# Performance work log

Measured on AMD Instinct MI355X. Metric: run time of the kernel, lower is better.

The kernel has to match this reference:

```python
import jax, jax.numpy as jnp
import numpy as np

G, T, S, M = 128, 512, 24, 4


def setup_inputs() -> dict:
    key = jax.random.key(0)
    k0, k1, k2, k3, k4 = jax.random.split(key, 5)
    inp = jax.random.normal(k0, (G, T, M), dtype=jnp.float32)
    # Stable-ish transition matrices: near 0.95*I
    F = 0.95 * jnp.eye(S, dtype=jnp.float32) + 0.05 * jax.random.normal(k1, (G, T, S, S), dtype=jnp.float32) / jnp.sqrt(S)
    # PSD process noise Q = c*A A^T + eps*I
    Aq = jax.random.normal(k2, (G, T, S, S), dtype=jnp.float32)
    Q = (0.01 / S) * jnp.einsum('gtik,gtjk->gtij', Aq, Aq) + 1e-3 * jnp.eye(S, dtype=jnp.float32)
    H = 0.5 * jax.random.normal(k3, (G, T, M, S), dtype=jnp.float32)
    # PSD measurement noise R
    Ar = jax.random.normal(k4, (G, T, M, M), dtype=jnp.float32)
    R = (0.1 / M) * jnp.einsum('gtik,gtjk->gtij', Ar, Ar) + 1e-2 * jnp.eye(M, dtype=jnp.float32)
    init_mean = jnp.zeros((G, S), dtype=jnp.float32)
    init_cov = jnp.broadcast_to(jnp.eye(S, dtype=jnp.float32), (G, S, S))
    return dict(input=inp, F=F, Q=Q, H=H, R=R, init_mean=init_mean, init_cov=init_cov)


def _measure(m, P, Hc, Rc):
    # one-step-ahead measurement distribution: mu = H m, Sig = H P H^T + R
    mu = jnp.einsum('gms,gs->gm', Hc, m)
    Sig = Hc @ P @ Hc.swapaxes(-1, -2) + Rc
    return mu, Sig


def _kalman(input, F, Q, H, R, init_mean, init_cov):
    # time-major for scan
    y = jnp.moveaxis(input, 1, 0)      # [T,G,M]
    Ft = jnp.moveaxis(F, 1, 0)         # [T,G,S,S]
    Qt = jnp.moveaxis(Q, 1, 0)
    Ht = jnp.moveaxis(H, 1, 0)         # [T,G,M,S]
    Rt = jnp.moveaxis(R, 1, 0)         # [T,G,M,M]

    mu0, Sig0 = _measure(init_mean, init_cov, Ht[0], Rt[0])

    def step(carry, x):
        m, P = carry                     # state prediction for t-1: [G,S], [G,S,S]
        yprev, Fp, Qp, Hp, Rp, Hc, Rc = x
        # --- update with obs at t-1 (using H,R from the t-1 measurement) ---
        HP = Hp @ P                      # [G,M,S]
        Sm = HP @ Hp.swapaxes(-1, -2) + Rp   # innovation cov [G,M,M]
        # K = P H^T S^{-1}; using symmetry: K = solve(S, H P)^T
        K = jnp.linalg.solve(Sm, HP).swapaxes(-1, -2)  # [G,S,M]
        resid = yprev - jnp.einsum('gms,gs->gm', Hp, m)
        m_u = m + jnp.einsum('gsm,gm->gs', K, resid)
        P_u = P - K @ HP
        # --- predict to t ---
        m_p = jnp.einsum('gij,gj->gi', Fp, m_u)
        P_p = Fp @ P_u @ Fp.swapaxes(-1, -2) + Qp
        # --- measurement at t ---
        mu, Sig = _measure(m_p, P_p, Hc, Rc)
        return (m_p, P_p), (mu, Sig)

    xs = (y[:-1], Ft[:-1], Qt[:-1], Ht[:-1], Rt[:-1], Ht[1:], Rt[1:])
    _, (mus, Sigs) = jax.lax.scan(step, (init_mean, init_cov), xs)
    means = jnp.moveaxis(jnp.concatenate([mu0[None], mus], axis=0), 0, 1)   # [G,T,M]
    covs = jnp.moveaxis(jnp.concatenate([Sig0[None], Sigs], axis=0), 0, 1)  # [G,T,M,M]
    return means, covs


def reference(input, F, Q, H, R, init_mean, init_cov):
    return _kalman(input, F, Q, H, R, init_mean, init_cov)
```

## Files before the change

kernel.cpp:

```cpp
#include <hip/hip_runtime.h>

#define Gn 128
#define Tn 512
#define Sn 24
#define SP 28
#define Mn 4
#define COVS_BASE (Gn * Tn * Mn)

__device__ __forceinline__ float4 ld4(const float* p) {
    return *reinterpret_cast<const float4*>(p);
}
__device__ __forceinline__ void st4(float* p, float4 v) {
    *reinterpret_cast<float4*>(p) = v;
}
__device__ __forceinline__ float dot4(float4 a, float4 b) {
    return a.x*b.x + a.y*b.y + a.z*b.z + a.w*b.w;
}

struct Row24 { float4 v[6]; };

__device__ __forceinline__ Row24 loadRow(const float* p) {
    Row24 r;
#pragma unroll
    for (int i = 0; i < 6; ++i) r.v[i] = ld4(p + 4*i);
    return r;
}

__device__ __forceinline__ float dot24(const Row24& a, const float* b) {
    float4 b0 = ld4(b+0), b1 = ld4(b+4), b2 = ld4(b+8),
           b3 = ld4(b+12), b4 = ld4(b+16), b5 = ld4(b+20);
    float s0 = a.v[0].x*b0.x + a.v[0].y*b0.y + a.v[0].z*b0.z + a.v[0].w*b0.w;
    float s1 = a.v[1].x*b1.x + a.v[1].y*b1.y + a.v[1].z*b1.z + a.v[1].w*b1.w;
    float s2 = a.v[2].x*b2.x + a.v[2].y*b2.y + a.v[2].z*b2.z + a.v[2].w*b2.w;
    float s3 = a.v[3].x*b3.x + a.v[3].y*b3.y + a.v[3].z*b3.z + a.v[3].w*b3.w;
    float s4 = a.v[4].x*b4.x + a.v[4].y*b4.y + a.v[4].z*b4.z + a.v[4].w*b4.w;
    float s5 = a.v[5].x*b5.x + a.v[5].y*b5.y + a.v[5].z*b5.z + a.v[5].w*b5.w;
    return ((s0+s1)+(s2+s3))+(s4+s5);
}

__device__ __forceinline__ void barrierLds() {
    asm volatile("s_waitcnt lgkmcnt(0)" ::: "memory");
    __builtin_amdgcn_s_barrier();
    asm volatile("" ::: "memory");
}
__device__ __forceinline__ void waveLds() {
    asm volatile("s_waitcnt lgkmcnt(0)" ::: "memory");
    __builtin_amdgcn_wave_barrier();
    asm volatile("" ::: "memory");
}

extern "C" __global__ void __launch_bounds__(256)
kalman_kernel(const float* __restrict__ y_g, const float* __restrict__ F_g,
              const float* __restrict__ Q_g, const float* __restrict__ H_g,
              const float* __restrict__ R_g, const float* __restrict__ m0_g,
              const float* __restrict__ P0_g, float* __restrict__ out)
{
    const int g   = blockIdx.x;
    const int tid = threadIdx.x;
    const int gT  = g * Tn;

    __shared__ __align__(16) float sP[Sn*SP];
    __shared__ __align__(16) float sPu[Sn*SP];
    __shared__ __align__(16) float sTmp[Sn*SP];
    __shared__ __align__(16) float sF[2][Sn*SP];
    __shared__ __align__(16) float sQ[2][Sn*SP];
    __shared__ __align__(16) float sH[2][Mn*SP];
    __shared__ __align__(16) float sR[2][16];
    __shared__ __align__(16) float sy[2][4];
    __shared__ __align__(16) float sHP[Mn*SP];
    __shared__ __align__(16) float sHPT[Sn*4];
    __shared__ __align__(16) float sK[Sn*4];
    __shared__ __align__(16) float sSig[16];
    __shared__ __align__(16) float sInv[16];
    __shared__ __align__(16) float sMean[Sn];
    __shared__ __align__(16) float sMu_[Sn];
    __shared__ __align__(16) float sResid[4];

    const float4* F4 = reinterpret_cast<const float4*>(F_g);
    const float4* Q4 = reinterpret_cast<const float4*>(Q_g);
    const float4* H4 = reinterpret_cast<const float4*>(H_g);
    const float4* R4 = reinterpret_cast<const float4*>(R_g);
    const float4* y4 = reinterpret_cast<const float4*>(y_g);

    auto stage_load = [&](int v, int t) -> float4 {
        if (v < 144)      return F4[(gT + t)*144 + v];
        else if (v < 288) return Q4[(gT + t)*144 + (v-144)];
        else if (v < 312) return H4[(gT + t)*24  + (v-288)];
        else if (v < 316) return R4[(gT + t)*4   + (v-312)];
        else              return y4[gT + t];
    };
    auto stage_store = [&](int v, int bb, float4 val) {
        if (v < 144)      { int r = v/6,        c = (v%6)*4;       st4(&sF[bb][r*SP+c], val); }
        else if (v < 288) { int v2 = v-144; int r = v2/6, c = (v2%6)*4; st4(&sQ[bb][r*SP+c], val); }
        else if (v < 312) { int v2 = v-288; int r = v2/6, c = (v2%6)*4; st4(&sH[bb][r*SP+c], val); }
        else if (v < 316) { st4(&sR[bb][(v-312)*4], val); }
        else              { st4(&sy[bb][0], val); }
    };

    if (tid < 144) {
        int r = tid / 6, c = (tid % 6) * 4;
        st4(&sP[r*SP + c], ld4(&P0_g[g*Sn*Sn + tid*4]));
    } else if (tid < 150) {
        int v = tid - 144;
        st4(&sMean[v*4], ld4(&m0_g[g*Sn + v*4]));
    }
    {
        float4 a0 = stage_load(tid, 0);
        stage_store(tid, 0, a0);
        if (tid + 256 < 317) {
            float4 a1 = stage_load(tid + 256, 0);
            stage_store(tid + 256, 0, a1);
        }
    }
    barrierLds();

    float4 pf0, pf1;

    for (int t = 0; t < Tn; ++t) {
        const int  b    = t & 1;
        const int  b1   = b ^ 1;
        const bool last = (t == Tn - 1);

        if (!last) {
            pf0 = stage_load(tid, t+1);
            if (tid + 256 < 317) pf1 = stage_load(tid + 256, t+1);
        }
        if (tid < 96) {
            int a = tid / 24, s = tid % 24;
            Row24 hr = loadRow(&sH[b][a*SP]);
            float hp = dot24(hr, &sP[s*SP]);
            sHP[a*SP + s]  = hp;
            sHPT[s*4 + a]  = hp;
        } else if (tid >= 128 && tid < 132) {
            int a = tid - 128;
            Row24 hr = loadRow(&sH[b][a*SP]);
            float mu = dot24(hr, sMean);
            out[(gT + t)*4 + a] = mu;
            sResid[a] = sy[b][a] - mu;
        }
        barrierLds();

        if (tid < 64) {
            if (tid < 16) {
                int a = tid >> 2, c = tid & 3;
                Row24 hpr = loadRow(&sHP[a*SP]);
                float sig = dot24(hpr, &sH[b][c*SP]) + sR[b][tid];
                sSig[tid] = sig;
                out[COVS_BASE + (size_t)(gT + t)*16 + tid] = sig;
            }
            if (!last) {
                waveLds();
                if (tid < 16) {
                    float s00=sSig[0],  s01=sSig[1],  s02=sSig[2],  s03=sSig[3];
                    float s10=sSig[4],  s11=sSig[5],  s12=sSig[6],  s13=sSig[7];
                    float s20=sSig[8],  s21=sSig[9],  s22=sSig[10], s23=sSig[11];
                    float s30=sSig[12], s31=sSig[13], s32=sSig[14], s33=sSig[15];
                    float p0 = s00*s11 - s01*s10;
                    float p1 = s00*s12 - s02*s10;
                    float p2 = s00*s13 - s03*s10;
                    float p3 = s01*s12 - s02*s11;
                    float p4 = s01*s13 - s03*s11;
                    float p5 = s02*s13 - s03*s12;
                    float q0c = s20*s31 - s21*s30;
                    float q1c = s20*s32 - s22*s30;
                    float q2c = s20*s33 - s23*s30;
                    float q3c = s21*s32 - s22*s31;
                    float q4c = s21*s33 - s23*s31;
                    float q5c = s22*s33 - s23*s32;
                    float det  = p0*q5c - p1*q4c + p2*q3c + p3*q2c - p4*q1c + p5*q0c;
                    float rdet = 1.0f / det;
                    int ia = tid >> 2, ic = tid & 3;
                    int r0 = (ic==0)?1:0, r1 = (ic<=1)?2:1, r2 = (ic<=2)?3:2;
                    int u0 = (ia==0)?1:0, u1 = (ia<=1)?2:1, u2 = (ia<=2)?3:2;
                    float m00=sSig[r0*4+u0], m01=sSig[r0*4+u1], m02=sSig[r0*4+u2];
                    float m10=sSig[r1*4+u0], m11=sSig[r1*4+u1], m12=sSig[r1*4+u2];
                    float m20=sSig[r2*4+u0], m21=sSig[r2*4+u1], m22=sSig[r2*4+u2];
                    float minor = m00*(m11*m22 - m12*m21)
                                - m01*(m10*m22 - m12*m20)
                                + m02*(m10*m21 - m11*m20);
                    float cof = ((ia + ic) & 1) ? -minor : minor;
                    sInv[tid] = cof * rdet;
                }
                waveLds();
                {
                    int a = tid / 24, s = tid % 24;
                    float kt = dot4(ld4(&sInv[a*4]), ld4(&sHPT[s*4]));
                    sK[s*4 + a] = kt;
                    if (tid < 32) {
                        int o2 = 64 + tid, a3 = o2/24, s3 = o2%24;
                        float kt2 = dot4(ld4(&sInv[a3*4]), ld4(&sHPT[s3*4]));
                        sK[s3*4 + a3] = kt2;
                    }
                }
            }
        }
        if (last) return;
        barrierLds();

        {
            int o = 2*tid, i = o/24, j = o%24;
            float4 kr = ld4(&sK[i*4]);
            float pu0 = sP[i*SP+j]   - dot4(kr, ld4(&sHPT[j*4]));
            float pu1 = sP[i*SP+j+1] - dot4(kr, ld4(&sHPT[(j+1)*4]));
            sPu[i*SP+j]   = pu0;
            sPu[i*SP+j+1] = pu1;
            if (tid >= 64 && tid < 128) {
                int o2 = 512 + (tid-64), i2 = o2/24, j2 = o2%24;
                sPu[i2*SP+j2] = sP[i2*SP+j2] - dot4(ld4(&sK[i2*4]), ld4(&sHPT[j2*4]));
            }
            if (tid >= 192 && tid < 216) {
                int s = tid - 192;
                sMu_[s] = sMean[s] + dot4(ld4(&sK[s*4]), ld4(&sResid[0]));
            }
        }
        barrierLds();

        {
            int o = 2*tid, i = o/24, j = o%24;
            Row24 fr = loadRow(&sF[b][i*SP]);
            sTmp[i*SP+j]   = dot24(fr, &sPu[j*SP]);
            sTmp[i*SP+j+1] = dot24(fr, &sPu[(j+1)*SP]);
            if (tid >= 64 && tid < 128) {
                int o2 = 512 + (tid-64), i2 = o2/24, j2 = o2%24;
                Row24 fr2 = loadRow(&sF[b][i2*SP]);
                sTmp[i2*SP+j2] = dot24(fr2, &sPu[j2*SP]);
            }
            if (tid >= 224 && tid < 248) {
                int i3 = tid - 224;
                Row24 fr3 = loadRow(&sF[b][i3*SP]);
                sMean[i3] = dot24(fr3, sMu_);
            }
        }
        barrierLds();

        {
            int o = 2*tid, i = o/24, j = o%24;
            Row24 tr = loadRow(&sTmp[i*SP]);
            sP[i*SP+j]   = dot24(tr, &sF[b][j*SP])     + sQ[b][i*SP+j];
            sP[i*SP+j+1] = dot24(tr, &sF[b][(j+1)*SP]) + sQ[b][i*SP+j+1];
            if (tid >= 64 && tid < 128) {
                int o2 = 512 + (tid-64), i2 = o2/24, j2 = o2%24;
                Row24 tr2 = loadRow(&sTmp[i2*SP]);
                sP[i2*SP+j2] = dot24(tr2, &sF[b][j2*SP]) + sQ[b][i2*SP+j2];
            }
            stage_store(tid, b1, pf0);
            if (tid + 256 < 317) stage_store(tid + 256, b1, pf1);
        }
        barrierLds();
    }
}

extern "C" void kernel_launch(void* const* d_in, const int* in_sizes, int n_in,
                              void* d_out, int out_size, void* d_ws, size_t ws_size,
                              hipStream_t stream) {
    kalman_kernel<<<Gn, 256, 0, stream>>>(
        (const float*)d_in[0], (const float*)d_in[1], (const float*)d_in[2],
        (const float*)d_in[3], (const float*)d_in[4], (const float*)d_in[5],
        (const float*)d_in[6], (float*)d_out);
}
```

Measured before the change: 1.282 ms.

## Reformulate Kalman step algebraically to cut per-step barriers from five to three

Rewrites the covariance update as F P F^T + Q - V S^{-1} V^T, where V = F P H^T, and the mean update as F m + V S^{-1} resid. This removes the explicit gain K and the intermediate P_u/Tmp matrices. F·P is now computed alongside H·P, and V, F·m and the 4x4 inverse are computed in parallel on different waves. The goal is to cut barrier-separated phases per time step and shorten the serial dependency chain. It changes the floating-point ordering of the covariance update and could be slightly less numerically stable than the Joseph-free K form.

```diff
diff --git a/kernel.cpp b/kernel.cpp
--- a/kernel.cpp
+++ b/kernel.cpp
@@ -60,21 +60,20 @@
     const int gT  = g * Tn;
 
     __shared__ __align__(16) float sP[Sn*SP];
-    __shared__ __align__(16) float sPu[Sn*SP];
-    __shared__ __align__(16) float sTmp[Sn*SP];
+    __shared__ __align__(16) float sG[Sn*SP];
     __shared__ __align__(16) float sF[2][Sn*SP];
     __shared__ __align__(16) float sQ[2][Sn*SP];
     __shared__ __align__(16) float sH[2][Mn*SP];
     __shared__ __align__(16) float sR[2][16];
     __shared__ __align__(16) float sy[2][4];
     __shared__ __align__(16) float sHP[Mn*SP];
-    __shared__ __align__(16) float sHPT[Sn*4];
-    __shared__ __align__(16) float sK[Sn*4];
-    __shared__ __align__(16) float sSig[16];
+    __shared__ __align__(16) float sV[Sn*4];
+    __shared__ __align__(16) float sSm[16];
     __shared__ __align__(16) float sInv[16];
     __shared__ __align__(16) float sMean[Sn];
-    __shared__ __align__(16) float sMu_[Sn];
+    __shared__ __align__(16) float sFm[Sn];
     __shared__ __align__(16) float sResid[4];
+    __shared__ __align__(16) float sr2[4];
 
     const float4* F4 = reinterpret_cast<const float4*>(F_g);
     const float4* Q4 = reinterpret_cast<const float4*>(Q_g);
@@ -90,7 +89,7 @@
         else              return y4[gT + t];
     };
     auto stage_store = [&](int v, int bb, float4 val) {
-        if (v < 144)      { int r = v/6,        c = (v%6)*4;       st4(&sF[bb][r*SP+c], val); }
+        if (v < 144)      { int r = v/6,        c = (v%6)*4;           st4(&sF[bb][r*SP+c], val); }
         else if (v < 288) { int v2 = v-144; int r = v2/6, c = (v2%6)*4; st4(&sQ[bb][r*SP+c], val); }
         else if (v < 312) { int v2 = v-288; int r = v2/6, c = (v2%6)*4; st4(&sH[bb][r*SP+c], val); }
         else if (v < 316) { st4(&sR[bb][(v-312)*4], val); }
@@ -107,7 +106,7 @@
     {
         float4 a0 = stage_load(tid, 0);
         stage_store(tid, 0, a0);
-        if (tid + 256 < 317) {
+        if (tid < 61) {
             float4 a1 = stage_load(tid + 256, 0);
             stage_store(tid + 256, 0, a1);
         }
@@ -123,38 +122,85 @@
 
         if (!last) {
             pf0 = stage_load(tid, t+1);
-            if (tid + 256 < 317) pf1 = stage_load(tid + 256, t+1);
+            if (tid < 61) pf1 = stage_load(tid + 256, t+1);
         }
         if (tid < 96) {
             int a = tid / 24, s = tid % 24;
             Row24 hr = loadRow(&sH[b][a*SP]);
-            float hp = dot24(hr, &sP[s*SP]);
-            sHP[a*SP + s]  = hp;
-            sHPT[s*4 + a]  = hp;
-        } else if (tid >= 128 && tid < 132) {
-            int a = tid - 128;
+            sHP[a*SP + s] = dot24(hr, &sP[s*SP]);
+        } else if (tid < 100) {
+            int a = tid - 96;
             Row24 hr = loadRow(&sH[b][a*SP]);
             float mu = dot24(hr, sMean);
             out[(gT + t)*4 + a] = mu;
             sResid[a] = sy[b][a] - mu;
+        } else if (!last) {
+            int o0 = 3*(tid - 100);
+            int i = o0/24, j0 = o0%24;
+            Row24 fr = loadRow(&sF[b][i*SP]);
+#pragma unroll
+            for (int d = 0; d < 3; ++d) {
+                sG[i*SP + j0 + d] = dot24(fr, &sP[(j0+d)*SP]);
+            }
         }
         barrierLds();
 
         if (tid < 64) {
-            if (tid < 16) {
-                int a = tid >> 2, c = tid & 3;
+            if (!last) {
+                if (tid < 32) {
+                    int v0 = 3*tid;
+                    int a = v0/24, i0 = v0%24;
+                    Row24 hpr = loadRow(&sHP[a*SP]);
+#pragma unroll
+                    for (int d = 0; d < 3; ++d) {
+                        int i = i0 + d;
+                        sV[i*4 + a] = dot24(hpr, &sF[b][i*SP]);
+                    }
+                } else if (tid < 40) {
+                    int i0 = 3*(tid - 32);
+#pragma unroll
+                    for (int d = 0; d < 3; ++d) {
+                        int i = i0 + d;
+                        Row24 fr = loadRow(&sF[b][i*SP]);
+                        sFm[i] = dot24(fr, sMean);
+                    }
+                } else {
+                    int o0 = 468 + 3*(tid - 40);
+                    int i = o0/24, j0 = o0%24;
+                    Row24 fr = loadRow(&sF[b][i*SP]);
+#pragma unroll
+                    for (int d = 0; d < 3; ++d) {
+                        sG[i*SP + j0 + d] = dot24(fr, &sP[(j0+d)*SP]);
+                    }
+                }
+            }
+        } else if (tid < 128) {
+            if (!last && tid < 76) {
+                int o0 = 540 + 3*(tid - 64);
+                int i = o0/24, j0 = o0%24;
+                Row24 fr = loadRow(&sF[b][i*SP]);
+#pragma unroll
+                for (int d = 0; d < 3; ++d) {
+                    sG[i*SP + j0 + d] = dot24(fr, &sP[(j0+d)*SP]);
+                }
+            }
+        } else if (tid < 192) {
+            if (tid < 144) {
+                int idx = tid - 128;
+                int a = idx >> 2, c = idx & 3;
                 Row24 hpr = loadRow(&sHP[a*SP]);
-                float sig = dot24(hpr, &sH[b][c*SP]) + sR[b][tid];
-                sSig[tid] = sig;
-                out[COVS_BASE + (size_t)(gT + t)*16 + tid] = sig;
+                float sig = dot24(hpr, &sH[b][c*SP]) + sR[b][idx];
+                sSm[idx] = sig;
+                out[COVS_BASE + (size_t)(gT + t)*16 + idx] = sig;
             }
             if (!last) {
                 waveLds();
-                if (tid < 16) {
-                    float s00=sSig[0],  s01=sSig[1],  s02=sSig[2],  s03=sSig[3];
-                    float s10=sSig[4],  s11=sSig[5],  s12=sSig[6],  s13=sSig[7];
-                    float s20=sSig[8],  s21=sSig[9],  s22=sSig[10], s23=sSig[11];
-                    float s30=sSig[12], s31=sSig[13], s32=sSig[14], s33=sSig[15];
+                if (tid < 144) {
+                    int idx = tid - 128;
+                    float s00=sSm[0],  s01=sSm[1],  s02=sSm[2],  s03=sSm[3];
+                    float s10=sSm[4],  s11=sSm[5],  s12=sSm[6],  s13=sSm[7];
+                    float s20=sSm[8],  s21=sSm[9],  s22=sSm[10], s23=sSm[11];
+                    float s30=sSm[12], s31=sSm[13], s32=sSm[14], s33=sSm[15];
                     float p0 = s00*s11 - s01*s10;
                     float p1 = s00*s12 - s02*s10;
                     float p2 = s00*s13 - s03*s10;
@@ -169,83 +215,53 @@
                     float q5c = s22*s33 - s23*s32;
                     float det  = p0*q5c - p1*q4c + p2*q3c + p3*q2c - p4*q1c + p5*q0c;
                     float rdet = 1.0f / det;
-                    int ia = tid >> 2, ic = tid & 3;
-                    int r0 = (ic==0)?1:0, r1 = (ic<=1)?2:1, r2 = (ic<=2)?3:2;
+                    int ia = idx >> 2, ic = idx & 3;
+                    int r0 = (ic==0)?1:0, r1 = (ic<=1)?2:1, r2i = (ic<=2)?3:2;
                     int u0 = (ia==0)?1:0, u1 = (ia<=1)?2:1, u2 = (ia<=2)?3:2;
-                    float m00=sSig[r0*4+u0], m01=sSig[r0*4+u1], m02=sSig[r0*4+u2];
-                    float m10=sSig[r1*4+u0], m11=sSig[r1*4+u1], m12=sSig[r1*4+u2];
-                    float m20=sSig[r2*4+u0], m21=sSig[r2*4+u1], m22=sSig[r2*4+u2];
+                    float m00=sSm[r0*4+u0], m01=sSm[r0*4+u1], m02=sSm[r0*4+u2];
+                    float m10=sSm[r1*4+u0], m11=sSm[r1*4+u1], m12=sSm[r1*4+u2];
+                    float m20=sSm[r2i*4+u0], m21=sSm[r2i*4+u1], m22=sSm[r2i*4+u2];
                     float minor = m00*(m11*m22 - m12*m21)
                                 - m01*(m10*m22 - m12*m20)
                                 + m02*(m10*m21 - m11*m20);
                     float cof = ((ia + ic) & 1) ? -minor : minor;
-                    sInv[tid] = cof * rdet;
+                    sInv[idx] = cof * rdet;
                 }
                 waveLds();
-                {
-                    int a = tid / 24, s = tid % 24;
-                    float kt = dot4(ld4(&sInv[a*4]), ld4(&sHPT[s*4]));
-                    sK[s*4 + a] = kt;
-                    if (tid < 32) {
-                        int o2 = 64 + tid, a3 = o2/24, s3 = o2%24;
-                        float kt2 = dot4(ld4(&sInv[a3*4]), ld4(&sHPT[s3*4]));
-                        sK[s3*4 + a3] = kt2;
-                    }
+                if (tid < 132) {
+                    int a = tid - 128;
+                    sr2[a] = dot4(ld4(&sInv[a*4]), ld4(&sResid[0]));
                 }
             }
         }
         if (last) return;
         barrierLds();
 
-        {
-            int o = 2*tid, i = o/24, j = o%24;
-            float4 kr = ld4(&sK[i*4]);
-            float pu0 = sP[i*SP+j]   - dot4(kr, ld4(&sHPT[j*4]));
-            float pu1 = sP[i*SP+j+1] - dot4(kr, ld4(&sHPT[(j+1)*4]));
-            sPu[i*SP+j]   = pu0;
-            sPu[i*SP+j+1] = pu1;
-            if (tid >= 64 && tid < 128) {
-                int o2 = 512 + (tid-64), i2 = o2/24, j2 = o2%24;
-                sPu[i2*SP+j2] = sP[i2*SP+j2] - dot4(ld4(&sK[i2*4]), ld4(&sHPT[j2*4]));
-            }
-            if (tid >= 192 && tid < 216) {
-                int s = tid - 192;
-                sMu_[s] = sMean[s] + dot4(ld4(&sK[s*4]), ld4(&sResid[0]));
-            }
-        }
-        barrierLds();
-
-        {
-            int o = 2*tid, i = o/24, j = o%24;
-            Row24 fr = loadRow(&sF[b][i*SP]);
-            sTmp[i*SP+j]   = dot24(fr, &sPu[j*SP]);
-            sTmp[i*SP+j+1] = dot24(fr, &sPu[(j+1)*SP]);
-            if (tid >= 64 && tid < 128) {
-                int o2 = 512 + (tid-64), i2 = o2/24, j2 = o2%24;
-                Row24 fr2 = loadRow(&sF[b][i2*SP]);
-                sTmp[i2*SP+j2] = dot24(fr2, &sPu[j2*SP]);
-            }
-            if (tid >= 224 && tid < 248) {
-                int i3 = tid - 224;
-                Row24 fr3 = loadRow(&sF[b][i3*SP]);
-                sMean[i3] = dot24(fr3, sMu_);
-            }
-        }
-        barrierLds();
-
-        {
-            int o = 2*tid, i = o/24, j = o%24;
-            Row24 tr = loadRow(&sTmp[i*SP]);
-            sP[i*SP+j]   = dot24(tr, &sF[b][j*SP])     + sQ[b][i*SP+j];
-            sP[i*SP+j+1] = dot24(tr, &sF[b][(j+1)*SP]) + sQ[b][i*SP+j+1];
-            if (tid >= 64 && tid < 128) {
-                int o2 = 512 + (tid-64), i2 = o2/24, j2 = o2%24;
-                Row24 tr2 = loadRow(&sTmp[i2*SP]);
-                sP[i2*SP+j2] = dot24(tr2, &sF[b][j2*SP]) + sQ[b][i2*SP+j2];
-            }
-            stage_store(tid, b1, pf0);
-            if (tid + 256 < 317) stage_store(tid + 256, b1, pf1);
-        }
+        if (tid < 192) {
+            int o0 = 3*tid;
+            int i = o0/24, j0 = o0%24;
+            Row24 gr = loadRow(&sG[i*SP]);
+            float4 vi   = ld4(&sV[i*4]);
+            float4 inv0 = ld4(&sInv[0]),  inv1 = ld4(&sInv[4]);
+            float4 inv2 = ld4(&sInv[8]),  inv3 = ld4(&sInv[12]);
+#pragma unroll
+            for (int d = 0; d < 3; ++d) {
+                int j = j0 + d;
+                float4 vj = ld4(&sV[j*4]);
+                float4 tj;
+                tj.x = dot4(inv0, vj);
+                tj.y = dot4(inv1, vj);
+                tj.z = dot4(inv2, vj);
+                tj.w = dot4(inv3, vj);
+                float val = dot24(gr, &sF[b][j*SP]) + sQ[b][i*SP + j] - dot4(vi, tj);
+                sP[i*SP + j] = val;
+            }
+        } else if (tid < 216) {
+            int s = tid - 192;
+            sMean[s] = sFm[s] + dot4(ld4(&sV[s*4]), ld4(&sr2[0]));
+        }
+        stage_store(tid, b1, pf0);
+        if (tid < 61) stage_store(tid + 256, b1, pf1);
         barrierLds();
     }
 }
```

After: 1.571 ms. 22.5% more time.
